# Performance work log

Hardware: AMD Instinct MI355X
Metric: run time of the kernel (lower is better)

## Reference

```python
import jax, jax.numpy as jnp
import numpy as np

DIM = 1024
NUM_HEADS = 16
HEAD_DIM = DIM // NUM_HEADS
SCALE = HEAD_DIM ** -0.5


def setup_inputs() -> dict:
    key = jax.random.key(0)
    ks = jax.random.split(key, 12)
    B, N, M, C = 4, 512, 2048, DIM
    x = jax.random.normal(ks[0], (B, N, C), dtype=jnp.float32)
    context = jax.random.normal(ks[1], (B, M, C), dtype=jnp.float32)
    mask = jax.random.randint(ks[2], (B, M), 0, 2, dtype=jnp.int32)
    mask = mask.at[:, 0].set(1)  # ensure at least one valid key per row
    w = 0.02
    Wq = jax.random.normal(ks[3], (C, C), dtype=jnp.float32) * w
    bq = jnp.zeros((C,), dtype=jnp.float32)
    Wk = jax.random.normal(ks[4], (C, C), dtype=jnp.float32) * w
    bk = jnp.zeros((C,), dtype=jnp.float32)
    Wv = jax.random.normal(ks[5], (C, C), dtype=jnp.float32) * w
    bv = jnp.zeros((C,), dtype=jnp.float32)
    Wo = jax.random.normal(ks[6], (C, C), dtype=jnp.float32) * w
    bo = jnp.zeros((C,), dtype=jnp.float32)
    return {"x": x, "context": context, "ctx_key_padding_mask": mask,
            "Wq": Wq, "bq": bq, "Wk": Wk, "bk": bk,
            "Wv": Wv, "bv": bv, "Wo": Wo, "bo": bo}


def reference(x, context, ctx_key_padding_mask, Wq, bq, Wk, bk, Wv, bv, Wo, bo):
    B, N, C = x.shape
    M = context.shape[1]
    H, D = NUM_HEADS, HEAD_DIM
    # torch nn.Linear: y = x @ W.T + b
    q = (x @ Wq.T + bq).reshape(B, N, H, D)
    k = (context @ Wk.T + bk).reshape(B, M, H, D)
    v = (context @ Wv.T + bv).reshape(B, M, H, D)
    scores = jnp.einsum('bnhd,bmhd->bhnm', q, k) * SCALE  # [B,H,N,M]
    neg = jnp.finfo(scores.dtype).min
    bias = jnp.where(ctx_key_padding_mask[:, None, None, :] != 0, 0.0, neg).astype(scores.dtype)
    attn = jax.nn.softmax(scores + bias, axis=-1)
    out = jnp.einsum('bhnm,bmhd->bnhd', attn, v).reshape(B, N, C)
    return out @ Wo.T + bo
```

## Files before the change

kernel.cpp:

```cpp
#include <hip/hip_runtime.h>
#include <hip/hip_bf16.h>
#include <stdint.h>


typedef __attribute__((ext_vector_type(4))) float f32x4;
typedef __attribute__((ext_vector_type(8))) __bf16 bf16x8;
typedef __attribute__((ext_vector_type(8))) unsigned short u16x8;

#define DEVI __device__ __forceinline__

#define QSC (0.125f * 1.44269504088896f)

DEVI f32x4 mfma16(u16x8 a, u16x8 b, f32x4 c) {
  return __builtin_amdgcn_mfma_f32_16x16x32_bf16(
      __builtin_bit_cast(bf16x8, a), __builtin_bit_cast(bf16x8, b), c, 0, 0, 0);
}

DEVI unsigned short f2bf(float f) {
  union { float f; unsigned int u; } x; x.f = f;
  unsigned int u = x.u;
  return (unsigned short)((u + 0x7fffu + ((u >> 16) & 1u)) >> 16);
}

DEVI float exp2_fast(float x) {
#if __has_builtin(__builtin_amdgcn_exp2f)
  return __builtin_amdgcn_exp2f(x);
#else
  return exp2f(x);
#endif
}

DEVI void llds16(const void* g, void* l) {
  __builtin_amdgcn_global_load_lds(
      (const __attribute__((address_space(1))) void*)g,
      (__attribute__((address_space(3))) void*)l, 16, 0, 0);
}

__global__ __launch_bounds__(256)
void cast_fused(const float* __restrict__ x, const float* __restrict__ ctx,
                const float* __restrict__ wq, const float* __restrict__ wk,
                const float* __restrict__ wv, const float* __restrict__ wo,
                const int* __restrict__ mask,
                unsigned short* __restrict__ xb, unsigned short* __restrict__ cb,
                unsigned short* __restrict__ wqb, unsigned short* __restrict__ wkb,
                unsigned short* __restrict__ wvb, unsigned short* __restrict__ wob) {
  int bid = blockIdx.x;
  const int tid = threadIdx.x;
  if (bid >= 2048 && bid < 10240) {
    __shared__ int red[256][2];
    int r = bid - 2048;
    int b = r >> 11, i = r & 2047;
    const int* mb = mask + b * 2048;
    int sall = 0, spre = 0;
#pragma unroll
    for (int j = 0; j < 8; ++j) {
      int p = tid * 8 + j;
      int v = (mb[p] != 0);
      sall += v;
      spre += (p < i) ? v : 0;
    }
    red[tid][0] = spre; red[tid][1] = sall;
    __syncthreads();
    for (int off = 128; off > 0; off >>= 1) {
      if (tid < off) { red[tid][0] += red[tid + off][0]; red[tid][1] += red[tid + off][1]; }
      __syncthreads();
    }
    const int pre = red[0][0], c = red[0][1];
    const int valid = (mb[i] != 0);
    int dst;
    if (valid) {
      dst = pre;
    } else {
      dst = c + (i - pre);
      if (dst >= ((c + 255) & ~255)) return;
    }
    unsigned short* dp = cb + ((size_t)(b * 2048 + dst)) * 1024 + tid * 4;
    if (valid) {
      const float4 v = *(const float4*)(ctx + ((size_t)(b * 2048 + i)) * 1024 + tid * 4);
      ushort4 o;
      o.x = f2bf(v.x); o.y = f2bf(v.y); o.z = f2bf(v.z); o.w = f2bf(v.w);
      *(ushort4*)dp = o;
    } else {
      ushort4 z; z.x = z.y = z.z = z.w = 0;
      *(ushort4*)dp = z;
    }
    return;
  }
  const float* src; unsigned short* dst; float scale = 1.f;
  if (bid < 2048)        { src = x;   dst = xb; }
  else if (bid < 11264)  { src = wq;  dst = wqb; bid -= 10240; scale = QSC; }
  else if (bid < 12288)  { src = wk;  dst = wkb; bid -= 11264; }
  else if (bid < 13312)  { src = wv;  dst = wvb; bid -= 12288; }
  else                   { src = wo;  dst = wob; bid -= 13312; }
  int e = (bid * 256 + tid) * 4;
  const float4 v = *(const float4*)(src + e);
  ushort4 o;
  o.x = f2bf(v.x * scale); o.y = f2bf(v.y * scale);
  o.z = f2bf(v.z * scale); o.w = f2bf(v.w * scale);
  *(ushort4*)(dst + e) = o;
}

DEVI void epi_store(f32x4 (&acc)[4][4], const float* __restrict__ bias,
                    float bscale, void* __restrict__ Cout,
                    int bm, int bn, int logS, int mode,
                    unsigned short* cst, int tid, int wave, int l15, int quad) {
  const int wm = wave & 1, wn = wave >> 1;
  __syncthreads();
  for (int half = 0; half < 2; ++half) {
    if (wm == half) {
#pragma unroll
      for (int mi = 0; mi < 4; ++mi)
#pragma unroll
        for (int ni = 0; ni < 4; ++ni)
#pragma unroll
          for (int r = 0; r < 4; ++r) {
            int lrow = mi * 16 + quad * 4 + r;
            int lcol = wn * 64 + ni * 16 + l15;
            unsigned short bv = f2bf(acc[mi][ni][r] + bias[bn + lcol] * bscale);
            if (mode == 0) cst[lrow * 136 + lcol] = bv;
            else           cst[lcol * 72 + lrow] = bv;
          }
    }
    __syncthreads();
    if (mode == 0) {
      int lrow = tid >> 2, cc = (tid & 3) * 32;
      int row = bm + half * 64 + lrow;
      int S = 1 << logS;
      int b = row >> logS, sl = row & (S - 1);
#pragma unroll
      for (int j = 0; j < 4; ++j) {
        int col = bn + cc + j * 8;
        int h = col >> 6, d8 = (col & 63) >> 3;
        size_t base = (((size_t)(b * 16 + h)) << logS) * 64 +
                      (size_t)(sl >> 4) * 1024 + d8 * 128 + (sl & 15) * 8;
        *(u16x8*)&((unsigned short*)Cout)[base] =
            *(const u16x8*)&cst[lrow * 136 + cc + j * 8];
      }
    } else {
      int c = tid >> 1, rc = (tid & 1) * 32;
      int gc = bn + c, h = gc >> 6, d = gc & 63;
      int b = bm >> 11;
#pragma unroll
      for (int j = 0; j < 4; ++j) {
        int key = (bm & 2047) + half * 64 + rc + j * 8;
        size_t base = (size_t)(b * 16 + h) * 131072 +
                      (size_t)(((key >> 6) * 4 + (d >> 4)) * 8 + ((key >> 3) & 7)) * 128 +
                      (d & 15) * 8;
        *(u16x8*)&((unsigned short*)Cout)[base] =
            *(const u16x8*)&cst[c * 72 + rc + j * 8];
      }
    }
    __syncthreads();
  }
}

DEVI void kv_body(const unsigned short* __restrict__ A,
                  const unsigned short* __restrict__ WK,
                  const unsigned short* __restrict__ WV,
                  const float* __restrict__ bk, const float* __restrict__ bv,
                  unsigned short* __restrict__ kh, unsigned short* __restrict__ vt,
                  int bm, int bn, unsigned short* sh) {
  constexpr int K = 1024;
  unsigned short* As = sh;
  unsigned short* Ks = sh + 128 * 64;
  unsigned short* Vs = sh + 2 * 128 * 64;

  const int tid = threadIdx.x;
  const int wave = tid >> 6, lane = tid & 63;
  const int l15 = lane & 15, quad = lane >> 4;
  const int wm = wave & 1, wn = wave >> 1;

  f32x4 ak[4][4] = {}, av[4][4] = {};

  for (int k0 = 0; k0 < K; k0 += 64) {
    __syncthreads();
#pragma unroll
    for (int c = 0; c < 4; ++c) {
      int s = c * 256 + tid;
      int m = s >> 3;
      int k8 = (s & 7) ^ (m & 7);
      llds16(A + (size_t)(bm + m) * K + k0 + k8 * 8, &As[s * 8]);
      llds16(WK + (size_t)(bn + m) * K + k0 + k8 * 8, &Ks[s * 8]);
      llds16(WV + (size_t)(bn + m) * K + k0 + k8 * 8, &Vs[s * 8]);
    }
    __syncthreads();
#pragma unroll
    for (int ks = 0; ks < 2; ++ks) {
      const int k8 = ks * 4 + quad;
      u16x8 af[4], bf[4];
#pragma unroll
      for (int i = 0; i < 4; ++i) {
        int m = wm * 64 + i * 16 + l15;
        af[i] = *(const u16x8*)(&As[(m * 8 + (k8 ^ (m & 7))) * 8]);
      }
#pragma unroll
      for (int i = 0; i < 4; ++i) {
        int n = wn * 64 + i * 16 + l15;
        bf[i] = *(const u16x8*)(&Ks[(n * 8 + (k8 ^ (n & 7))) * 8]);
      }
#pragma unroll
      for (int mi = 0; mi < 4; ++mi)
#pragma unroll
        for (int ni = 0; ni < 4; ++ni)
          ak[mi][ni] = mfma16(af[mi], bf[ni], ak[mi][ni]);
#pragma unroll
      for (int i = 0; i < 4; ++i) {
        int n = wn * 64 + i * 16 + l15;
        bf[i] = *(const u16x8*)(&Vs[(n * 8 + (k8 ^ (n & 7))) * 8]);
      }
#pragma unroll
      for (int mi = 0; mi < 4; ++mi)
#pragma unroll
        for (int ni = 0; ni < 4; ++ni)
          av[mi][ni] = mfma16(af[mi], bf[ni], av[mi][ni]);
    }
  }

  epi_store(ak, bk, 1.f, kh, bm, bn, 11, 0, sh, tid, wave, l15, quad);
  epi_store(av, bv, 1.f, vt, bm, bn, 11, 2, sh, tid, wave, l15, quad);
}

DEVI void q_body(const unsigned short* __restrict__ A,
                 const unsigned short* __restrict__ W,
                 const float* __restrict__ bias,
                 unsigned short* __restrict__ Cout,
                 int bm, int bn, unsigned short* sh) {
  constexpr int K = 1024;
  unsigned short* As = sh;
  unsigned short* Bs = sh + 128 * 64;

  const int tid = threadIdx.x;
  const int wave = tid >> 6, lane = tid & 63;
  const int l15 = lane & 15, quad = lane >> 4;
  const int wm = wave & 1, wn = wave >> 1;

  f32x4 acc[4][4] = {};

  for (int k0 = 0; k0 < K; k0 += 64) {
    __syncthreads();
#pragma unroll
    for (int c = 0; c < 4; ++c) {
      int s = c * 256 + tid;
      int m = s >> 3;
      int k8 = (s & 7) ^ (m & 7);
      llds16(A + (size_t)(bm + m) * K + k0 + k8 * 8, &As[s * 8]);
      llds16(W + (size_t)(bn + m) * K + k0 + k8 * 8, &Bs[s * 8]);
    }
    __syncthreads();
#pragma unroll
    for (int ks = 0; ks < 2; ++ks) {
      const int k8 = ks * 4 + quad;
      u16x8 af[4], bf[4];
#pragma unroll
      for (int i = 0; i < 4; ++i) {
        int m = wm * 64 + i * 16 + l15;
        af[i] = *(const u16x8*)(&As[(m * 8 + (k8 ^ (m & 7))) * 8]);
        int n = wn * 64 + i * 16 + l15;
        bf[i] = *(const u16x8*)(&Bs[(n * 8 + (k8 ^ (n & 7))) * 8]);
      }
#pragma unroll
      for (int mi = 0; mi < 4; ++mi)
#pragma unroll
        for (int ni = 0; ni < 4; ++ni)
          acc[mi][ni] = mfma16(af[mi], bf[ni], acc[mi][ni]);
    }
  }

  epi_store(acc, bias, QSC, Cout, bm, bn, 9, 0, sh, tid, wave, l15, quad);
}

__global__ __launch_bounds__(256, 2)
void gemm_qkv(const unsigned short* __restrict__ xb,
              const unsigned short* __restrict__ cb,
              const unsigned short* __restrict__ wq,
              const unsigned short* __restrict__ wk,
              const unsigned short* __restrict__ wv,
              const float* __restrict__ bq, const float* __restrict__ bk,
              const float* __restrict__ bv,
              const int* __restrict__ mask,
              unsigned short* __restrict__ qh, unsigned short* __restrict__ kh,
              unsigned short* __restrict__ vt) {
  __shared__ __align__(16) unsigned short sh[128 * 64 * 3];
  __shared__ int qsum[260];
  const int id = blockIdx.x;
  const int tid = threadIdx.x;

  {
    int s = 0;
    const int* mp = mask + tid * 32;
#pragma unroll 8
    for (int j = 0; j < 32; ++j) s += (mp[j] != 0);
    qsum[tid] = s;
    __syncthreads();
    if (tid < 4) {
      int tot = 0;
      for (int k = 0; k < 64; ++k) tot += qsum[tid * 64 + k];
      qsum[256 + tid] = tot;
    }
    __syncthreads();
  }
  const int nb0 = ((qsum[256] + 255) & ~255) >> 7;
  const int nb1 = ((qsum[257] + 255) & ~255) >> 7;
  const int nb2 = ((qsum[258] + 255) & ~255) >> 7;
  const int nb3 = ((qsum[259] + 255) & ~255) >> 7;
  const int L = nb0 + nb1 + nb2 + nb3;
  if (id < L * 8) {
    int xl = id >> 3, y = id & 7, b = 0;
    if (xl >= nb0) { xl -= nb0; b = 1;
      if (xl >= nb1) { xl -= nb1; b = 2;
        if (xl >= nb2) { xl -= nb2; b = 3; } } }
    kv_body(cb, wk, wv, bk, bv, kh, vt, b * 2048 + xl * 128, y * 128, sh);
  } else if (id < L * 8 + 128) {
    const int q = id - L * 8;
    q_body(xb, wq, bq, qh, (q & 15) * 128, (q >> 4) * 128, sh);
  }
}

__global__ __launch_bounds__(256)
void gemm_o(const unsigned short* __restrict__ A,
            const unsigned short* __restrict__ W,
            const float* __restrict__ bo, float* __restrict__ out) {
  constexpr int K = 1024;
  __shared__ __align__(16) unsigned short As[64 * 64];
  __shared__ __align__(16) unsigned short Bs[128 * 64];

  const int tid = threadIdx.x;
  const int wave = tid >> 6, lane = tid & 63;
  const int l15 = lane & 15, quad = lane >> 4;
  const int bm = blockIdx.x * 64, bn = blockIdx.y * 128;

  f32x4 acc[4][2] = {};

  for (int k0 = 0; k0 < K; k0 += 64) {
    __syncthreads();
#pragma unroll
    for (int c = 0; c < 2; ++c) {
      int s = c * 256 + tid;
      int m = s >> 3, k8 = (s & 7) ^ (m & 7);
      llds16(A + (size_t)(bm + m) * K + k0 + k8 * 8, &As[s * 8]);
    }
#pragma unroll
    for (int c = 0; c < 4; ++c) {
      int s = c * 256 + tid;
      int m = s >> 3, k8 = (s & 7) ^ (m & 7);
      llds16(W + (size_t)(bn + m) * K + k0 + k8 * 8, &Bs[s * 8]);
    }
    __syncthreads();
#pragma unroll
    for (int ks = 0; ks < 2; ++ks) {
      const int k8 = ks * 4 + quad;
      u16x8 af[4], bf[2];
#pragma unroll
      for (int i = 0; i < 4; ++i) {
        int m = i * 16 + l15;
        af[i] = *(const u16x8*)(&As[(m * 8 + (k8 ^ (m & 7))) * 8]);
      }
#pragma unroll
      for (int i = 0; i < 2; ++i) {
        int n = wave * 32 + i * 16 + l15;
        bf[i] = *(const u16x8*)(&Bs[(n * 8 + (k8 ^ (n & 7))) * 8]);
      }
#pragma unroll
      for (int mi = 0; mi < 4; ++mi)
#pragma unroll
        for (int ni = 0; ni < 2; ++ni)
          acc[mi][ni] = mfma16(af[mi], bf[ni], acc[mi][ni]);
    }
  }

#pragma unroll
  for (int mi = 0; mi < 4; ++mi)
#pragma unroll
    for (int ni = 0; ni < 2; ++ni)
#pragma unroll
      for (int r = 0; r < 4; ++r) {
        int row = bm + mi * 16 + quad * 4 + r;
        int col = bn + wave * 32 + ni * 16 + l15;
        out[(size_t)row * 1024 + col] = acc[mi][ni][r] + bo[col];
      }
}

#define PS 72
__global__ __launch_bounds__(256, 2)
void attn_kernel(const unsigned short* __restrict__ Q,
                 const unsigned short* __restrict__ K,
                 const unsigned short* __restrict__ Vt,
                 const int* __restrict__ mask,
                 unsigned short* __restrict__ O) {
  __shared__ __align__(16) unsigned short p_lds[4][2][16 * PS];
  __shared__ float l_lds[4][64];
  __shared__ __align__(16) float o_comb[64][68];
  __shared__ int wsum[4];

  const int tid = threadIdx.x;
  const int wave = tid >> 6, lane = tid & 63;
  const int l15 = lane & 15, quad = lane >> 4;
  const int bh = blockIdx.x, b = bh >> 4, h = bh & 15;
  const int q0 = blockIdx.y * 64;

  {
    const int* mb = mask + b * 2048;
    int s = 0;
#pragma unroll
    for (int j = 0; j < 8; ++j) s += (mb[tid * 8 + j] != 0);
#pragma unroll
    for (int off = 1; off < 64; off <<= 1) s += __shfl_xor(s, off, 64);
    if (lane == 0) wsum[wave] = s;
    __syncthreads();
  }
  const int c = wsum[0] + wsum[1] + wsum[2] + wsum[3];
  const int T = (c + 255) >> 8;

  const unsigned short* Qb = Q + (size_t)bh * 32768 + (size_t)(q0 >> 4) * 1024;
  const unsigned short* Kb = K + (size_t)bh * 131072;
  const unsigned short* Vb = Vt + (size_t)bh * 131072;

  u16x8 aq[4][2];
#pragma unroll
  for (int qg = 0; qg < 4; ++qg)
#pragma unroll
    for (int ks = 0; ks < 2; ++ks)
      aq[qg][ks] = *(const u16x8*)(Qb + ((qg * 8 + ks * 4 + quad) * 16 + l15) * 8);

  f32x4 o_acc[4][4] = {};
  float l_s[4] = {0.f, 0.f, 0.f, 0.f};

  u16x8 kf[2][4];

  auto load_k = [&](int kb) {
    const int kg0 = kb >> 4;
#pragma unroll
    for (int ns = 0; ns < 4; ++ns)
#pragma unroll
      for (int ks = 0; ks < 2; ++ks)
        kf[ks][ns] = *(const u16x8*)(Kb + (((size_t)(kg0 + ns) * 8 + ks * 4 + quad) * 16 + l15) * 8);
  };

  load_k(wave * 64);

#pragma unroll 1
  for (int t = 0; t < T; ++t) {
    const int kb = wave * 64 + t * 256;
    const int kb_next = kb + (t + 1 < T ? 256 : 0);

    u16x8 vf[2][4];
    const int kt4 = (kb >> 6) * 4;
#pragma unroll
    for (int nd = 0; nd < 4; ++nd)
#pragma unroll
      for (int ks = 0; ks < 2; ++ks)
        vf[ks][nd] = *(const u16x8*)(Vb + (((size_t)(kt4 + nd) * 8 + ks * 4 + quad) * 16 + l15) * 8);

    f32x4 bfr[4];
    if (kb + 64 <= c) {
#pragma unroll
      for (int ns = 0; ns < 4; ++ns)
        bfr[ns] = f32x4{-8.f, -8.f, -8.f, -8.f};
    } else {
#pragma unroll
      for (int ns = 0; ns < 4; ++ns)
#pragma unroll
        for (int r = 0; r < 4; ++r)
          bfr[ns][r] = (kb + ns * 16 + quad * 4 + r < c) ? -8.f : -1e30f;
    }

#pragma unroll
    for (int qg = 0; qg < 4; ++qg) {
      f32x4 sfr[4];
#pragma unroll
      for (int ns = 0; ns < 4; ++ns) {
        f32x4 sa = bfr[ns];
#pragma unroll
        for (int ks = 0; ks < 2; ++ks)
          sa = mfma16(kf[ks][ns], aq[qg][ks], sa);
        sfr[ns] = sa;
      }

      if (qg == 3) load_k(kb_next);

      float rsum = 0.f;
#pragma unroll
      for (int ns = 0; ns < 4; ++ns) {
        unsigned int pr[4];
#pragma unroll
        for (int r = 0; r < 4; ++r) {
          float p = exp2_fast(sfr[ns][r]);
          unsigned int u = __builtin_bit_cast(unsigned int, p) & 0xffff0000u;
          rsum += __builtin_bit_cast(float, u);
          pr[r] = u;
        }
        uint2 pw;
        pw.x = __builtin_amdgcn_perm(pr[1], pr[0], 0x07060302u);
        pw.y = __builtin_amdgcn_perm(pr[3], pr[2], 0x07060302u);
        *(uint2*)&p_lds[wave][qg & 1][l15 * PS + ns * 16 + quad * 4] = pw;
      }
      rsum += __shfl_xor(rsum, 16, 64);
      rsum += __shfl_xor(rsum, 32, 64);
      l_s[qg] += rsum;

#pragma unroll
      for (int ks = 0; ks < 2; ++ks) {
        u16x8 pf = *(const u16x8*)&p_lds[wave][qg & 1][l15 * PS + ks * 32 + quad * 8];
#pragma unroll
        for (int nd = 0; nd < 4; ++nd)
          o_acc[qg][nd] = mfma16(pf, vf[ks][nd], o_acc[qg][nd]);
      }
    }
  }

  if (quad == 0) {
#pragma unroll
    for (int qg = 0; qg < 4; ++qg)
      l_lds[wave][qg * 16 + l15] = l_s[qg];
  }
  __syncthreads();

  for (int w = 0; w < 4; ++w) {
    if (wave == w) {
#pragma unroll
      for (int qg = 0; qg < 4; ++qg)
#pragma unroll
        for (int r = 0; r < 4; ++r) {
          const int q = qg * 16 + quad * 4 + r;
#pragma unroll
          for (int nd = 0; nd < 4; ++nd) {
            const int d = nd * 16 + l15;
            float v = o_acc[qg][nd][r];
            if (w == 0) o_comb[q][d] = v;
            else        o_comb[q][d] += v;
          }
        }
    }
    __syncthreads();
  }

  {
    const int q = tid >> 2, dc = (tid & 3) * 16;
    const float inv = 1.f / (l_lds[0][q] + l_lds[1][q] + l_lds[2][q] + l_lds[3][q]);
    unsigned short* Ob = O + ((size_t)(b * 512 + q0 + q)) * 1024 + h * 64 + dc;
    u16x8 o1, o2;
#pragma unroll
    for (int j = 0; j < 8; ++j) o1[j] = f2bf(o_comb[q][dc + j] * inv);
#pragma unroll
    for (int j = 0; j < 8; ++j) o2[j] = f2bf(o_comb[q][dc + 8 + j] * inv);
    *(u16x8*)(Ob) = o1;
    *(u16x8*)(Ob + 8) = o2;
  }
}

extern "C" void kernel_launch(void* const* d_in, const int* in_sizes, int n_in,
                              void* d_out, int out_size, void* d_ws, size_t ws_size,
                              hipStream_t stream) {
  const float* x   = (const float*)d_in[0];
  const float* ctx = (const float*)d_in[1];
  const int* mask  = (const int*)d_in[2];
  const float* Wq  = (const float*)d_in[3];
  const float* bq  = (const float*)d_in[4];
  const float* Wk  = (const float*)d_in[5];
  const float* bk  = (const float*)d_in[6];
  const float* Wv  = (const float*)d_in[7];
  const float* bv  = (const float*)d_in[8];
  const float* Wo  = (const float*)d_in[9];
  const float* bo  = (const float*)d_in[10];

  char* ws = (char*)d_ws;
  unsigned short* xb  = (unsigned short*)(ws + ((size_t)0  << 20));
  unsigned short* cb  = (unsigned short*)(ws + ((size_t)4  << 20));
  unsigned short* wqb = (unsigned short*)(ws + ((size_t)20 << 20));
  unsigned short* wkb = (unsigned short*)(ws + ((size_t)22 << 20));
  unsigned short* wvb = (unsigned short*)(ws + ((size_t)24 << 20));
  unsigned short* wob = (unsigned short*)(ws + ((size_t)26 << 20));
  unsigned short* qh  = (unsigned short*)(ws + ((size_t)28 << 20));
  unsigned short* kh  = (unsigned short*)(ws + ((size_t)32 << 20));
  unsigned short* vt  = (unsigned short*)(ws + ((size_t)48 << 20));
  unsigned short* ah  = (unsigned short*)(ws + ((size_t)64 << 20));

  cast_fused<<<14336, 256, 0, stream>>>(x, ctx, Wq, Wk, Wv, Wo, mask,
                                        xb, cb, wqb, wkb, wvb, wob);
  gemm_qkv<<<640, 256, 0, stream>>>(xb, cb, wqb, wkb, wvb,
                                    bq, bk, bv, mask, qh, kh, vt);
  attn_kernel<<<dim3(64, 8), 256, 0, stream>>>(qh, kh, vt, mask, ah);
  gemm_o<<<dim3(32, 8), 256, 0, stream>>>(ah, wob, bo, (float*)d_out);
}
```

Measured before the change: 192.0 us.

## Precompute mask prefix-sum metadata once and shrink cast kernel grid

Adds a small mask_meta kernel that computes a per-batch scan of the key padding mask, producing per-row compaction destinations and valid-key counts. The cast kernel, the QKV GEMM and the attention kernel then read these precomputed values. Previously each of the 8192 context-row blocks, every QKV block and every attention block recomputed the mask reductions. The cast kernel also processes four rows or four float4 chunks per block, cutting the grid from 14336 to 3584 blocks. The cost is one extra small kernel launch on the critical path.

Measured after the change: 187.0 us. 1.03x faster.

```diff
diff --git a/kernel.cpp b/kernel.cpp
--- a/kernel.cpp
+++ b/kernel.cpp
@@ -37,67 +37,90 @@
 }
 
 __global__ __launch_bounds__(256)
+void mask_meta(const int* __restrict__ mask, int* __restrict__ meta,
+               int* __restrict__ cnt) {
+  const int b = blockIdx.x;
+  const int tid = threadIdx.x;
+  const int* mb = mask + b * 2048;
+  int v[8], s = 0;
+#pragma unroll
+  for (int j = 0; j < 8; ++j) { v[j] = (mb[tid * 8 + j] != 0) ? 1 : 0; s += v[j]; }
+  __shared__ int sc[2][256];
+  sc[0][tid] = s;
+  __syncthreads();
+  int src = 0;
+  for (int off = 1; off < 256; off <<= 1) {
+    int x = sc[src][tid];
+    if (tid >= off) x += sc[src][tid - off];
+    sc[src ^ 1][tid] = x;
+    src ^= 1;
+    __syncthreads();
+  }
+  const int incl = sc[src][tid];
+  const int c = sc[src][255];
+  int pre = incl - s;
+#pragma unroll
+  for (int j = 0; j < 8; ++j) {
+    const int p = tid * 8 + j;
+    const unsigned dst = v[j] ? (unsigned)pre : (unsigned)(c + (p - pre));
+    meta[b * 2048 + p] = (int)(dst | (v[j] ? 0x80000000u : 0u));
+    pre += v[j];
+  }
+  if (tid == 0) cnt[b] = c;
+}
+
+__global__ __launch_bounds__(256)
 void cast_fused(const float* __restrict__ x, const float* __restrict__ ctx,
                 const float* __restrict__ wq, const float* __restrict__ wk,
                 const float* __restrict__ wv, const float* __restrict__ wo,
-                const int* __restrict__ mask,
+                const int* __restrict__ meta, const int* __restrict__ cnt,
                 unsigned short* __restrict__ xb, unsigned short* __restrict__ cb,
                 unsigned short* __restrict__ wqb, unsigned short* __restrict__ wkb,
                 unsigned short* __restrict__ wvb, unsigned short* __restrict__ wob) {
   int bid = blockIdx.x;
   const int tid = threadIdx.x;
-  if (bid >= 2048 && bid < 10240) {
-    __shared__ int red[256][2];
-    int r = bid - 2048;
-    int b = r >> 11, i = r & 2047;
-    const int* mb = mask + b * 2048;
-    int sall = 0, spre = 0;
-#pragma unroll
-    for (int j = 0; j < 8; ++j) {
-      int p = tid * 8 + j;
-      int v = (mb[p] != 0);
-      sall += v;
-      spre += (p < i) ? v : 0;
-    }
-    red[tid][0] = spre; red[tid][1] = sall;
-    __syncthreads();
-    for (int off = 128; off > 0; off >>= 1) {
-      if (tid < off) { red[tid][0] += red[tid + off][0]; red[tid][1] += red[tid + off][1]; }
-      __syncthreads();
-    }
-    const int pre = red[0][0], c = red[0][1];
-    const int valid = (mb[i] != 0);
-    int dst;
-    if (valid) {
-      dst = pre;
-    } else {
-      dst = c + (i - pre);
-      if (dst >= ((c + 255) & ~255)) return;
-    }
-    unsigned short* dp = cb + ((size_t)(b * 2048 + dst)) * 1024 + tid * 4;
-    if (valid) {
-      const float4 v = *(const float4*)(ctx + ((size_t)(b * 2048 + i)) * 1024 + tid * 4);
-      ushort4 o;
-      o.x = f2bf(v.x); o.y = f2bf(v.y); o.z = f2bf(v.z); o.w = f2bf(v.w);
-      *(ushort4*)dp = o;
-    } else {
-      ushort4 z; z.x = z.y = z.z = z.w = 0;
-      *(ushort4*)dp = z;
+  if (bid >= 512 && bid < 2560) {
+    const int r0 = (bid - 512) * 4;
+#pragma unroll
+    for (int rr = 0; rr < 4; ++rr) {
+      const int r = r0 + rr;
+      const int b = r >> 11;
+      const unsigned mv = (unsigned)meta[r];
+      const int valid = (int)(mv >> 31);
+      const int dst = (int)(mv & 0x7fffffffu);
+      if (!valid && dst >= ((cnt[b] + 255) & ~255)) continue;
+      unsigned short* dp = cb + ((size_t)(b * 2048 + dst)) * 1024 + tid * 4;
+      if (valid) {
+        const float4 v = *(const float4*)(ctx + ((size_t)r) * 1024 + tid * 4);
+        ushort4 o;
+        o.x = f2bf(v.x); o.y = f2bf(v.y); o.z = f2bf(v.z); o.w = f2bf(v.w);
+        *(ushort4*)dp = o;
+      } else {
+        ushort4 z; z.x = z.y = z.z = z.w = 0;
+        *(ushort4*)dp = z;
+      }
     }
     return;
   }
   const float* src; unsigned short* dst; float scale = 1.f;
-  if (bid < 2048)        { src = x;   dst = xb; }
-  else if (bid < 11264)  { src = wq;  dst = wqb; bid -= 10240; scale = QSC; }
-  else if (bid < 12288)  { src = wk;  dst = wkb; bid -= 11264; }
-  else if (bid < 13312)  { src = wv;  dst = wvb; bid -= 12288; }
-  else                   { src = wo;  dst = wob; bid -= 13312; }
-  int e = (bid * 256 + tid) * 4;
-  const float4 v = *(const float4*)(src + e);
-  ushort4 o;
-  o.x = f2bf(v.x * scale); o.y = f2bf(v.y * scale);
-  o.z = f2bf(v.z * scale); o.w = f2bf(v.w * scale);
-  *(ushort4*)(dst + e) = o;
+  if (bid < 512) { src = x; dst = xb; }
+  else {
+    bid -= 2560;
+    const int w = bid >> 8; bid &= 255;
+    src = (w == 0) ? wq : (w == 1) ? wk : (w == 2) ? wv : wo;
+    dst = (w == 0) ? wqb : (w == 1) ? wkb : (w == 2) ? wvb : wob;
+    if (w == 0) scale = QSC;
+  }
+  const int e0 = bid * 4096 + tid * 4;
+#pragma unroll
+  for (int it = 0; it < 4; ++it) {
+    const int e = e0 + it * 1024;
+    const float4 v = *(const float4*)(src + e);
+    ushort4 o;
+    o.x = f2bf(v.x * scale); o.y = f2bf(v.y * scale);
+    o.z = f2bf(v.z * scale); o.w = f2bf(v.w * scale);
+    *(ushort4*)(dst + e) = o;
+  }
 }
 
 DEVI void epi_store(f32x4 (&acc)[4][4], const float* __restrict__ bias,
@@ -277,32 +300,16 @@
               const unsigned short* __restrict__ wv,
               const float* __restrict__ bq, const float* __restrict__ bk,
               const float* __restrict__ bv,
-              const int* __restrict__ mask,
+              const int* __restrict__ cnt,
               unsigned short* __restrict__ qh, unsigned short* __restrict__ kh,
               unsigned short* __restrict__ vt) {
   __shared__ __align__(16) unsigned short sh[128 * 64 * 3];
-  __shared__ int qsum[260];
   const int id = blockIdx.x;
-  const int tid = threadIdx.x;
-
-  {
-    int s = 0;
-    const int* mp = mask + tid * 32;
-#pragma unroll 8
-    for (int j = 0; j < 32; ++j) s += (mp[j] != 0);
-    qsum[tid] = s;
-    __syncthreads();
-    if (tid < 4) {
-      int tot = 0;
-      for (int k = 0; k < 64; ++k) tot += qsum[tid * 64 + k];
-      qsum[256 + tid] = tot;
-    }
-    __syncthreads();
-  }
-  const int nb0 = ((qsum[256] + 255) & ~255) >> 7;
-  const int nb1 = ((qsum[257] + 255) & ~255) >> 7;
-  const int nb2 = ((qsum[258] + 255) & ~255) >> 7;
-  const int nb3 = ((qsum[259] + 255) & ~255) >> 7;
+
+  const int nb0 = ((cnt[0] + 255) & ~255) >> 7;
+  const int nb1 = ((cnt[1] + 255) & ~255) >> 7;
+  const int nb2 = ((cnt[2] + 255) & ~255) >> 7;
+  const int nb3 = ((cnt[3] + 255) & ~255) >> 7;
   const int L = nb0 + nb1 + nb2 + nb3;
   if (id < L * 8) {
     int xl = id >> 3, y = id & 7, b = 0;
@@ -385,12 +392,11 @@
 void attn_kernel(const unsigned short* __restrict__ Q,
                  const unsigned short* __restrict__ K,
                  const unsigned short* __restrict__ Vt,
-                 const int* __restrict__ mask,
+                 const int* __restrict__ cnt,
                  unsigned short* __restrict__ O) {
   __shared__ __align__(16) unsigned short p_lds[4][2][16 * PS];
   __shared__ float l_lds[4][64];
   __shared__ __align__(16) float o_comb[64][68];
-  __shared__ int wsum[4];
 
   const int tid = threadIdx.x;
   const int wave = tid >> 6, lane = tid & 63;
@@ -398,17 +404,7 @@
   const int bh = blockIdx.x, b = bh >> 4, h = bh & 15;
   const int q0 = blockIdx.y * 64;
 
-  {
-    const int* mb = mask + b * 2048;
-    int s = 0;
-#pragma unroll
-    for (int j = 0; j < 8; ++j) s += (mb[tid * 8 + j] != 0);
-#pragma unroll
-    for (int off = 1; off < 64; off <<= 1) s += __shfl_xor(s, off, 64);
-    if (lane == 0) wsum[wave] = s;
-    __syncthreads();
-  }
-  const int c = wsum[0] + wsum[1] + wsum[2] + wsum[3];
+  const int c = cnt[b];
   const int T = (c + 255) >> 8;
 
   const unsigned short* Qb = Q + (size_t)bh * 32768 + (size_t)(q0 >> 4) * 1024;
@@ -574,11 +570,14 @@
   unsigned short* kh  = (unsigned short*)(ws + ((size_t)32 << 20));
   unsigned short* vt  = (unsigned short*)(ws + ((size_t)48 << 20));
   unsigned short* ah  = (unsigned short*)(ws + ((size_t)64 << 20));
-
-  cast_fused<<<14336, 256, 0, stream>>>(x, ctx, Wq, Wk, Wv, Wo, mask,
-                                        xb, cb, wqb, wkb, wvb, wob);
+  int* meta           = (int*)(ws + ((size_t)68 << 20));
+  int* cntp           = meta + 8192;
+
+  mask_meta<<<4, 256, 0, stream>>>(mask, meta, cntp);
+  cast_fused<<<3584, 256, 0, stream>>>(x, ctx, Wq, Wk, Wv, Wo, meta, cntp,
+                                       xb, cb, wqb, wkb, wvb, wob);
   gemm_qkv<<<640, 256, 0, stream>>>(xb, cb, wqb, wkb, wvb,
-                                    bq, bk, bv, mask, qh, kh, vt);
-  attn_kernel<<<dim3(64, 8), 256, 0, stream>>>(qh, kh, vt, mask, ah);
+                                    bq, bk, bv, cntp, qh, kh, vt);
+  attn_kernel<<<dim3(64, 8), 256, 0, stream>>>(qh, kh, vt, cntp, ah);
   gemm_o<<<dim3(32, 8), 256, 0, stream>>>(ah, wob, bo, (float*)d_out);
 }
```
